# Optimization experiments

Hardware: AMD Instinct MI355X
Metric: run time of the kernel (lower is better)

## Reference

```python
import jax, jax.numpy as jnp
import numpy as np

H_NODE = 256
H_EDGE = 64
B = 8        # number of graphs
A_PER = 64   # anchors per graph
N_PER = 512  # nodes per graph
INF = 1000000.0
EPS = 1e-8
D_MIN, D_MAX = 0.0, 20.0  # _rbf defaults (gvp-style)


def setup_inputs() -> dict:
    key = jax.random.key(0)
    ks = jax.random.split(key, 16)
    h, he = H_NODE, H_EDGE
    n = lambda k, shp, s=1.0: jax.random.normal(k, shp, jnp.float32) * s
    return {
        "anchor_x": n(ks[0], (B * A_PER, 3), 10.0),
        "node_x": n(ks[1], (B * N_PER, 3), 10.0),
        "anchor_features": n(ks[2], (B * A_PER, h)),
        "node_features": n(ks[3], (B * N_PER, h)),
        "batch": jnp.repeat(jnp.arange(B, dtype=jnp.int32), N_PER),
        "anchor_batch": jnp.repeat(jnp.arange(B, dtype=jnp.int32), A_PER),
        "node_mask": (jax.random.uniform(ks[4], (B * N_PER,)) < 0.9).astype(jnp.float32),
        "Wq": n(ks[5], (h, h), h ** -0.5), "bq": jnp.zeros((h,), jnp.float32),
        "Wkv": n(ks[6], (2 * h, h + he), (h + he) ** -0.5), "bkv": jnp.zeros((2 * h,), jnp.float32),
        "ln1_g": jnp.ones((h,), jnp.float32), "ln1_b": jnp.zeros((h,), jnp.float32),
        "W1": n(ks[7], (2 * h, h), h ** -0.5), "b1": jnp.zeros((2 * h,), jnp.float32),
        "W2": n(ks[8], (2 * h, 2 * h), (2 * h) ** -0.5), "b2": jnp.zeros((2 * h,), jnp.float32),
        "W3": n(ks[9], (h, 2 * h), (2 * h) ** -0.5), "b3": jnp.zeros((h,), jnp.float32),
        "ln2_g": jnp.ones((h,), jnp.float32), "ln2_b": jnp.zeros((h,), jnp.float32),
    }


def _ln(x, g, b, eps=1e-5):
    m = x.mean(-1, keepdims=True)
    v = ((x - m) ** 2).mean(-1, keepdims=True)
    return (x - m) * jax.lax.rsqrt(v + eps) * g + b


def _forward(anchor_x, node_x, anchor_features, node_features, node_mask,
             Wq, bq, Wkv, bkv, ln1_g, ln1_b, W1, b1, W2, b2, W3, b3, ln2_g, ln2_b):
    h, he = H_NODE, H_EDGE
    # equal-sized graphs: reshape global tensors to [B, ., .] (batch ids are repeat(arange(B)))
    q = (anchor_features @ Wq.T + bq).reshape(B, A_PER, h)
    ax = anchor_x.reshape(B, A_PER, 3)
    nx = node_x.reshape(B, N_PER, 3)
    nf = node_features.reshape(B, N_PER, h)
    mask = node_mask.reshape(B, N_PER)

    # pairwise anchor->node distances; original adds scalar eps to the diff vector before the norm
    dist = jnp.linalg.norm(ax[:, :, None, :] - nx[:, None, :, :] + EPS, axis=-1)  # [B,A,N]

    # RBF featurization of dist/10 with D_count = h_edge
    mu = jnp.linspace(D_MIN, D_MAX, he)
    sigma = (D_MAX - D_MIN) / he
    rbf = jnp.exp(-(((dist / 10.0)[..., None] - mu) / sigma) ** 2)  # [B,A,N,he]

    # kv_node(cat([node_feat, rbf])) decomposed: node part computed once per node
    Wkv_n, Wkv_e = Wkv[:, :h], Wkv[:, h:]
    kv_n = nf @ Wkv_n.T + bkv                 # [B,N,2h]
    kv_e = rbf @ Wkv_e.T                      # [B,A,N,2h]
    kv = kv_n[:, None, :, :] + kv_e           # [B,A,N,2h]
    k, v = kv[..., :h], kv[..., h:]

    attn = jnp.einsum('bah,banh->ban', q, k)
    attn = attn * ((mask[:, None, :] - 1.0) * INF)  # faithful to original (multiplicative mask)
    attn = jax.nn.softmax(attn, axis=-1)
    upd = jnp.einsum('ban,banh->bah', attn, v).reshape(B * A_PER, h)

    af = _ln(anchor_features + upd, ln1_g, ln1_b)
    m = jax.nn.relu(af @ W1.T + b1)
    m = jax.nn.relu(m @ W2.T + b2)
    m = m @ W3.T + b3
    return _ln(af + m, ln2_g, ln2_b)


def reference(anchor_x, node_x, anchor_features, node_features, batch, anchor_batch, node_mask,
              Wq, bq, Wkv, bkv, ln1_g, ln1_b, W1, b1, W2, b2, W3, b3, ln2_g, ln2_b):
    # batch / anchor_batch encode equal-sized contiguous graphs; structure is baked into reshapes
    return _forward(anchor_x, node_x, anchor_features, node_features, node_mask,
                    Wq, bq, Wkv, bkv, ln1_g, ln1_b, W1, b1, W2, b2, W3, b3, ln2_g, ln2_b)
```

## Files before the change

kernel.cpp:

```cpp
#include <hip/hip_runtime.h>

#define H    256
#define HE   64
#define NPB  512
#define NA   512
#define MU_STEP (20.0f / 63.0f)
#define INV_SIG 3.2f
#define NF_LD4 65

__device__ __forceinline__ float wave_sum(float v) {
#pragma unroll
    for (int o = 32; o; o >>= 1) v += __shfl_xor(v, o, 64);
    return v;
}
__device__ __forceinline__ float wave_max(float v) {
#pragma unroll
    for (int o = 32; o; o >>= 1) v = fmaxf(v, __shfl_xor(v, o, 64));
    return v;
}
__device__ __forceinline__ float block_sum512(float v, float* red8, int t) {
    v = wave_sum(v);
    if ((t & 63) == 0) red8[t >> 6] = v;
    __syncthreads();
    v = red8[0] + red8[1] + red8[2] + red8[3]
      + red8[4] + red8[5] + red8[6] + red8[7];
    __syncthreads();
    return v;
}

__global__ void __launch_bounds__(512) fused_all(
    const float* __restrict__ anchor_x, const float* __restrict__ node_x,
    const float* __restrict__ anchor_f, const float* __restrict__ node_f,
    const float* __restrict__ node_mask,
    const float* __restrict__ Wq,  const float* __restrict__ bq,
    const float* __restrict__ Wkv, const float* __restrict__ bkv,
    const float* __restrict__ ln1_g, const float* __restrict__ ln1_b,
    const float* __restrict__ W1, const float* __restrict__ b1,
    const float* __restrict__ W2, const float* __restrict__ b2,
    const float* __restrict__ W3, const float* __restrict__ b3,
    const float* __restrict__ g2,  const float* __restrict__ bb2,
    float* __restrict__ out)
{
    const int bid = blockIdx.x;
    const int b  = bid & 7;
    const int pr = bid >> 3;
    const int aA = b * 64 + 2 * pr;
    const int aB = aA + 1;
    const int t  = threadIdx.x;
    const int th = t & 255, h = t >> 8;
    const int wv = t >> 6, l = t & 63;
    const int sub = l >> 4, kc16 = l & 15;

    __shared__ __align__(16) float nf_s[2][16 * NF_LD4 * 4];
    __shared__ __align__(16) float qWe_s[2][324];
    __shared__ float q_s[2][256];
    __shared__ float af_s[2][256];
    __shared__ float d10_s[2][NPB];
    __shared__ float mf_s[NPB];
    __shared__ float lg_s[2][NPB];
    __shared__ float w_s[2][NPB];
    __shared__ float snf_s[2][256], rj_s[2][64];
    __shared__ float red[512], red8[8];
    __shared__ int   idx_s[2][NPB];
    __shared__ int   cnt_s[2];

    if (t < 256) af_s[0][t]  = anchor_f[(size_t)aA * 256 + t];
    else         af_s[1][th] = anchor_f[(size_t)aB * 256 + th];
    if (t < 2) cnt_s[t] = 0;

    {
        float axA0 = anchor_x[3 * aA], axA1 = anchor_x[3 * aA + 1], axA2 = anchor_x[3 * aA + 2];
        float axB0 = anchor_x[3 * aB], axB1 = anchor_x[3 * aB + 1], axB2 = anchor_x[3 * aB + 2];
        int ng = b * NPB + t;
        float nx0 = node_x[3 * ng], nx1 = node_x[3 * ng + 1], nx2 = node_x[3 * ng + 2];
        float dx = axA0 - nx0 + 1e-8f, dy = axA1 - nx1 + 1e-8f, dz = axA2 - nx2 + 1e-8f;
        d10_s[0][t] = sqrtf(dx * dx + dy * dy + dz * dz) * 0.1f;
        dx = axB0 - nx0 + 1e-8f; dy = axB1 - nx1 + 1e-8f; dz = axB2 - nx2 + 1e-8f;
        d10_s[1][t] = sqrtf(dx * dx + dy * dy + dz * dz) * 0.1f;
        mf_s[t] = (node_mask[ng] - 1.0f) * 1000000.0f;
    }
    __syncthreads();

    const float4* src0 = (const float4*)(node_f + (size_t)(b * NPB) * 256);
    float4 rA = src0[t], rB = src0[t + 512];

    for (int pass = 0; pass < 8; ++pass) {
        int m = pass * 32 + wv * 4 + sub;
        const float* wr = Wq + (size_t)m * 256 + kc16;
        float aAc = 0.f, aBc = 0.f;
        for (int u = 0; u < 16; u += 8) {
            float w8[8];
#pragma unroll
            for (int v = 0; v < 8; ++v) w8[v] = wr[(u + v) * 16];
#pragma unroll
            for (int v = 0; v < 8; ++v) {
                int c = kc16 + (u + v) * 16;
                aAc = fmaf(w8[v], af_s[0][c], aAc);
                aBc = fmaf(w8[v], af_s[1][c], aBc);
            }
        }
#pragma unroll
        for (int o = 8; o >= 1; o >>= 1) {
            aAc += __shfl_xor(aAc, o, 64);
            aBc += __shfl_xor(aBc, o, 64);
        }
        if (kc16 == 0) {
            float bv = bq[m];
            q_s[0][m] = aAc + bv;
            q_s[1][m] = aBc + bv;
        }
    }
    __syncthreads();

    if (t < 320) {
        float aAc = 0.f, aBc = 0.f;
        for (int o = 0; o < 256; o += 8) {
            float w8[8];
#pragma unroll
            for (int u = 0; u < 8; ++u) w8[u] = Wkv[(size_t)(o + u) * 320 + t];
#pragma unroll
            for (int u = 0; u < 8; ++u) {
                aAc = fmaf(w8[u], q_s[0][o + u], aAc);
                aBc = fmaf(w8[u], q_s[1][o + u], aBc);
            }
        }
        qWe_s[0][t] = aAc;
        qWe_s[1][t] = aBc;
    }
    const int dA = (t >> 6) * NF_LD4 + (t & 63);
    const int dB = ((t >> 6) + 8) * NF_LD4 + (t & 63);
    {
        float4* dst = (float4*)(nf_s[0]);
        dst[dA] = rA; dst[dB] = rB;
    }
    float qbkA = block_sum512((t < 256) ? q_s[0][t] * bkv[t] : 0.f, red8, t);
    float qbkB = block_sum512((t < 256) ? q_s[1][t] * bkv[t] : 0.f, red8, t);

    const int n16 = t >> 5, kc = t & 31;
    const float4* qwA4 = (const float4*)qWe_s[0];
    const float4* qwB4 = (const float4*)qWe_s[1];
    const float4 q0A = qwA4[2 * kc], q1A = qwA4[2 * kc + 1];
    const float4 q0B = qwB4[2 * kc], q1B = qwB4[2 * kc + 1];
    const float qeA0 = qWe_s[0][256 + 2 * kc], qeA1 = qWe_s[0][257 + 2 * kc];
    const float qeB0 = qWe_s[1][256 + 2 * kc], qeB1 = qWe_s[1][257 + 2 * kc];
    const float mu0 = (2 * kc) * MU_STEP, mu1 = (2 * kc + 1) * MU_STEP;

    for (int tile = 0; tile < 32; ++tile) {
        if (tile < 31) {
            const float4* s2 = (const float4*)(node_f + (size_t)(b * NPB + (tile + 1) * 16) * 256);
            rA = s2[t]; rB = s2[t + 512];
        }

        const float4* nf4 = (const float4*)(nf_s[tile & 1]) + n16 * NF_LD4;
        float4 f0 = nf4[2 * kc], f1 = nf4[2 * kc + 1];
        float sA = q0A.x * f0.x + q0A.y * f0.y + q0A.z * f0.z + q0A.w * f0.w
                 + q1A.x * f1.x + q1A.y * f1.y + q1A.z * f1.z + q1A.w * f1.w;
        float sB = q0B.x * f0.x + q0B.y * f0.y + q0B.z * f0.z + q0B.w * f0.w
                 + q1B.x * f1.x + q1B.y * f1.y + q1B.z * f1.z + q1B.w * f1.w;

        const int n = tile * 16 + n16;
        const float dA10 = d10_s[0][n], dB10 = d10_s[1][n];
        {
            float u = (dA10 - mu0) * INV_SIG; sA = fmaf(qeA0, __expf(-u * u), sA);
            u = (dA10 - mu1) * INV_SIG;       sA = fmaf(qeA1, __expf(-u * u), sA);
            u = (dB10 - mu0) * INV_SIG;       sB = fmaf(qeB0, __expf(-u * u), sB);
            u = (dB10 - mu1) * INV_SIG;       sB = fmaf(qeB1, __expf(-u * u), sB);
        }
#pragma unroll
        for (int o = 1; o < 32; o <<= 1) {
            sA += __shfl_xor(sA, o, 64);
            sB += __shfl_xor(sB, o, 64);
        }
        if (kc == 0) {
            lg_s[0][n] = (sA + qbkA) * mf_s[n];
            lg_s[1][n] = (sB + qbkB) * mf_s[n];
        }

        if (tile < 31) {
            float4* dst = (float4*)(nf_s[(tile + 1) & 1]);
            dst[dA] = rA; dst[dB] = rB;
        }
        __syncthreads();
    }

    float lg0 = lg_s[h][th], lg1 = lg_s[h][th + 256];
    {
        float m = wave_max(fmaxf(lg0, lg1));
        if ((t & 63) == 0) red8[t >> 6] = m;
    }
    __syncthreads();
    float gm = fmaxf(fmaxf(red8[4 * h], red8[4 * h + 1]),
                     fmaxf(red8[4 * h + 2], red8[4 * h + 3]));
    __syncthreads();
    float e0 = __expf(lg0 - gm), e1 = __expf(lg1 - gm);
    w_s[h][th] = e0; w_s[h][th + 256] = e1;
    {
        float sm = wave_sum(e0 + e1);
        if ((t & 63) == 0) red8[t >> 6] = sm;
    }
    __syncthreads();
    float inv = 1.0f / (red8[4 * h] + red8[4 * h + 1] + red8[4 * h + 2] + red8[4 * h + 3]);

    if (e0 > 0.f) { int p = atomicAdd(&cnt_s[h], 1); idx_s[h][p] = th; }
    if (e1 > 0.f) { int p = atomicAdd(&cnt_s[h], 1); idx_s[h][p] = th + 256; }
    __syncthreads();
    const int cnt = cnt_s[h];

    {
        float s = 0.f;
        const float* base = node_f + (size_t)(b * NPB) * 256 + th;
        for (int i = 0; i < cnt; ++i) {
            int n = idx_s[h][i];
            s += w_s[h][n] * base[(size_t)n * 256];
        }
        snf_s[h][th] = s;
    }
    {
        int j = th & 63, g = th >> 6;
        float mu = j * MU_STEP;
        float r = 0.f;
        for (int i = g; i < cnt; i += 4) {
            int n = idx_s[h][i];
            float uu = (d10_s[h][n] - mu) * INV_SIG;
            r += w_s[h][n] * __expf(-uu * uu);
        }
        red[t] = r;
    }
    __syncthreads();
    if (th < 64)
        rj_s[h][th] = red[h * 256 + th] + red[h * 256 + th + 64]
                    + red[h * 256 + th + 128] + red[h * 256 + th + 192];
    __syncthreads();

    for (int pass = 0; pass < 8; ++pass) {
        int m = pass * 32 + wv * 4 + sub;
        const float* wr = Wkv + (size_t)(256 + m) * 320 + kc16;
        float aAc = 0.f, aBc = 0.f;
        for (int u = 0; u < 16; u += 8) {
            float w8[8];
#pragma unroll
            for (int v = 0; v < 8; ++v) w8[v] = wr[(u + v) * 16];
#pragma unroll
            for (int v = 0; v < 8; ++v) {
                int c = kc16 + (u + v) * 16;
                aAc = fmaf(w8[v], snf_s[0][c], aAc);
                aBc = fmaf(w8[v], snf_s[1][c], aBc);
            }
        }
        {
            float w4r[4];
#pragma unroll
            for (int v = 0; v < 4; ++v) w4r[v] = wr[256 + v * 16];
#pragma unroll
            for (int v = 0; v < 4; ++v) {
                int j = kc16 + v * 16;
                aAc = fmaf(w4r[v], rj_s[0][j], aAc);
                aBc = fmaf(w4r[v], rj_s[1][j], aBc);
            }
        }
#pragma unroll
        for (int o = 8; o >= 1; o >>= 1) {
            aAc += __shfl_xor(aAc, o, 64);
            aBc += __shfl_xor(aBc, o, 64);
        }
        if (kc16 == 0) { red[m] = aAc; red[256 + m] = aBc; }
    }
    __syncthreads();

    float x = af_s[h][th] + red[h * 256 + th] * inv + bkv[256 + th];
    {
        float s1 = wave_sum(x);
        if ((t & 63) == 0) red8[t >> 6] = s1;
    }
    __syncthreads();
    float mean = (red8[4 * h] + red8[4 * h + 1] + red8[4 * h + 2] + red8[4 * h + 3]) * (1.0f / 256.0f);
    __syncthreads();
    float xc = x - mean;
    {
        float v1 = wave_sum(xc * xc);
        if ((t & 63) == 0) red8[t >> 6] = v1;
    }
    __syncthreads();
    float var = (red8[4 * h] + red8[4 * h + 1] + red8[4 * h + 2] + red8[4 * h + 3]) * (1.0f / 256.0f);
    __syncthreads();
    af_s[h][th] = xc * rsqrtf(var + 1e-5f) * ln1_g[th] + ln1_b[th];
    __syncthreads();

    float* mlp = (float*)nf_s;
    for (int pass = 0; pass < 16; ++pass) {
        int m = pass * 32 + wv * 4 + sub;
        const float* wr = W1 + (size_t)m * 256 + kc16;
        float aAc = 0.f, aBc = 0.f;
        for (int u = 0; u < 16; u += 8) {
            float w8[8];
#pragma unroll
            for (int v = 0; v < 8; ++v) w8[v] = wr[(u + v) * 16];
#pragma unroll
            for (int v = 0; v < 8; ++v) {
                int c = kc16 + (u + v) * 16;
                aAc = fmaf(w8[v], af_s[0][c], aAc);
                aBc = fmaf(w8[v], af_s[1][c], aBc);
            }
        }
#pragma unroll
        for (int o = 8; o >= 1; o >>= 1) {
            aAc += __shfl_xor(aAc, o, 64);
            aBc += __shfl_xor(aBc, o, 64);
        }
        if (kc16 == 0) {
            float bv = b1[m];
            mlp[m]       = fmaxf(aAc + bv, 0.f);
            mlp[512 + m] = fmaxf(aBc + bv, 0.f);
        }
    }
    __syncthreads();

    for (int pass = 0; pass < 16; ++pass) {
        int m = pass * 32 + wv * 4 + sub;
        const float* wr = W2 + (size_t)m * 512 + kc16;
        float aAc = 0.f, aBc = 0.f;
        for (int u = 0; u < 32; u += 8) {
            float w8[8];
#pragma unroll
            for (int v = 0; v < 8; ++v) w8[v] = wr[(u + v) * 16];
#pragma unroll
            for (int v = 0; v < 8; ++v) {
                int c = kc16 + (u + v) * 16;
                aAc = fmaf(w8[v], mlp[c], aAc);
                aBc = fmaf(w8[v], mlp[512 + c], aBc);
            }
        }
#pragma unroll
        for (int o = 8; o >= 1; o >>= 1) {
            aAc += __shfl_xor(aAc, o, 64);
            aBc += __shfl_xor(aBc, o, 64);
        }
        if (kc16 == 0) {
            float bv = b2[m];
            mlp[1024 + m] = fmaxf(aAc + bv, 0.f);
            mlp[1536 + m] = fmaxf(aBc + bv, 0.f);
        }
    }
    __syncthreads();

    for (int pass = 0; pass < 8; ++pass) {
        int m = pass * 32 + wv * 4 + sub;
        const float* wr = W3 + (size_t)m * 512 + kc16;
        float aAc = 0.f, aBc = 0.f;
        for (int u = 0; u < 32; u += 8) {
            float w8[8];
#pragma unroll
            for (int v = 0; v < 8; ++v) w8[v] = wr[(u + v) * 16];
#pragma unroll
            for (int v = 0; v < 8; ++v) {
                int c = kc16 + (u + v) * 16;
                aAc = fmaf(w8[v], mlp[1024 + c], aAc);
                aBc = fmaf(w8[v], mlp[1536 + c], aBc);
            }
        }
#pragma unroll
        for (int o = 8; o >= 1; o >>= 1) {
            aAc += __shfl_xor(aAc, o, 64);
            aBc += __shfl_xor(aBc, o, 64);
        }
        if (kc16 == 0) {
            float bv = b3[m];
            red[m]       = aAc + bv;
            red[256 + m] = aBc + bv;
        }
    }
    __syncthreads();

    const int kh = t >> 8;
    float yA = 0.f, yB = 0.f, gv = 0.f, bv2 = 0.f;
    if (kh == 0) {
        yA = red[th] + af_s[0][th];
        yB = red[256 + th] + af_s[1][th];
        gv = g2[th]; bv2 = bb2[th];
    }
    {
        float s  = block_sum512((kh == 0) ? yA : 0.f, red8, t);
        float mn = s * (1.0f / 256.0f);
        float yc = (kh == 0) ? (yA - mn) : 0.f;
        float vr = block_sum512(yc * yc, red8, t) * (1.0f / 256.0f);
        if (kh == 0)
            out[(size_t)aA * 256 + th] = yc * rsqrtf(vr + 1e-5f) * gv + bv2;
    }
    {
        float s  = block_sum512((kh == 0) ? yB : 0.f, red8, t);
        float mn = s * (1.0f / 256.0f);
        float yc = (kh == 0) ? (yB - mn) : 0.f;
        float vr = block_sum512(yc * yc, red8, t) * (1.0f / 256.0f);
        if (kh == 0)
            out[(size_t)aB * 256 + th] = yc * rsqrtf(vr + 1e-5f) * gv + bv2;
    }
}

extern "C" void kernel_launch(void* const* d_in, const int* in_sizes, int n_in,
                              void* d_out, int out_size, void* d_ws, size_t ws_size,
                              hipStream_t stream)
{
    const float* anchor_x  = (const float*)d_in[0];
    const float* node_x    = (const float*)d_in[1];
    const float* anchor_f  = (const float*)d_in[2];
    const float* node_f    = (const float*)d_in[3];
    const float* node_mask = (const float*)d_in[6];
    const float* Wq        = (const float*)d_in[7];
    const float* bq        = (const float*)d_in[8];
    const float* Wkv       = (const float*)d_in[9];
    const float* bkv       = (const float*)d_in[10];
    const float* ln1_g     = (const float*)d_in[11];
    const float* ln1_b     = (const float*)d_in[12];
    const float* W1        = (const float*)d_in[13];
    const float* b1        = (const float*)d_in[14];
    const float* W2        = (const float*)d_in[15];
    const float* b2        = (const float*)d_in[16];
    const float* W3        = (const float*)d_in[17];
    const float* b3        = (const float*)d_in[18];
    const float* ln2_g     = (const float*)d_in[19];
    const float* ln2_b     = (const float*)d_in[20];

    fused_all<<<256, 512, 0, stream>>>(anchor_x, node_x, anchor_f, node_f,
                                       node_mask, Wq, bq, Wkv, bkv,
                                       ln1_g, ln1_b, W1, b1, W2, b2, W3, b3,
                                       ln2_g, ln2_b, (float*)d_out);
}
```

Measured before the change: 172.9 us.

## Double block size to 1024 threads and stream node features directly from global

Raises the block from 512 to 1024 threads and redistributes every phase (Wq, Wkv projections, logits, softmax, weighted sums, MLP, layernorms) across 16 waves, halving the pass count per GEMV. The logit loop drops the shared-memory double-buffered node-feature tile and instead has each wave read one node row per iteration from global with a register prefetch, doing a full 64-lane shuffle reduction. The MLP intermediates move to dedicated shared arrays. This aims for more parallelism per block, at the cost of more registers per thread, more idle threads in some phases, and uncoalesced-per-wave node loads that rely on cache.

```diff
diff --git a/kernel.cpp b/kernel.cpp
--- a/kernel.cpp
+++ b/kernel.cpp
@@ -6,7 +6,6 @@
 #define NA   512
 #define MU_STEP (20.0f / 63.0f)
 #define INV_SIG 3.2f
-#define NF_LD4 65
 
 __device__ __forceinline__ float wave_sum(float v) {
 #pragma unroll
@@ -18,17 +17,18 @@
     for (int o = 32; o; o >>= 1) v = fmaxf(v, __shfl_xor(v, o, 64));
     return v;
 }
-__device__ __forceinline__ float block_sum512(float v, float* red8, int t) {
+__device__ __forceinline__ float block_sum1024(float v, float* red16, int t) {
     v = wave_sum(v);
-    if ((t & 63) == 0) red8[t >> 6] = v;
-    __syncthreads();
-    v = red8[0] + red8[1] + red8[2] + red8[3]
-      + red8[4] + red8[5] + red8[6] + red8[7];
+    if ((t & 63) == 0) red16[t >> 6] = v;
+    __syncthreads();
+    v = 0.f;
+#pragma unroll
+    for (int i = 0; i < 16; ++i) v += red16[i];
     __syncthreads();
     return v;
 }
 
-__global__ void __launch_bounds__(512) fused_all(
+__global__ void __launch_bounds__(1024) fused_all(
     const float* __restrict__ anchor_x, const float* __restrict__ node_x,
     const float* __restrict__ anchor_f, const float* __restrict__ node_f,
     const float* __restrict__ node_mask,
@@ -47,11 +47,9 @@
     const int aA = b * 64 + 2 * pr;
     const int aB = aA + 1;
     const int t  = threadIdx.x;
-    const int th = t & 255, h = t >> 8;
     const int wv = t >> 6, l = t & 63;
     const int sub = l >> 4, kc16 = l & 15;
 
-    __shared__ __align__(16) float nf_s[2][16 * NF_LD4 * 4];
     __shared__ __align__(16) float qWe_s[2][324];
     __shared__ float q_s[2][256];
     __shared__ float af_s[2][256];
@@ -60,15 +58,16 @@
     __shared__ float lg_s[2][NPB];
     __shared__ float w_s[2][NPB];
     __shared__ float snf_s[2][256], rj_s[2][64];
-    __shared__ float red[512], red8[8];
+    __shared__ float m1_s[2][512], m2_s[2][512];
+    __shared__ float red[512], red16[16];
     __shared__ int   idx_s[2][NPB];
     __shared__ int   cnt_s[2];
 
-    if (t < 256) af_s[0][t]  = anchor_f[(size_t)aA * 256 + t];
-    else         af_s[1][th] = anchor_f[(size_t)aB * 256 + th];
+    if (t < 256)       af_s[0][t]        = anchor_f[(size_t)aA * 256 + t];
+    else if (t < 512)  af_s[1][t - 256]  = anchor_f[(size_t)aB * 256 + (t - 256)];
     if (t < 2) cnt_s[t] = 0;
 
-    {
+    if (t < 512) {
         float axA0 = anchor_x[3 * aA], axA1 = anchor_x[3 * aA + 1], axA2 = anchor_x[3 * aA + 2];
         float axB0 = anchor_x[3 * aB], axB1 = anchor_x[3 * aB + 1], axB2 = anchor_x[3 * aB + 2];
         int ng = b * NPB + t;
@@ -81,11 +80,9 @@
     }
     __syncthreads();
 
-    const float4* src0 = (const float4*)(node_f + (size_t)(b * NPB) * 256);
-    float4 rA = src0[t], rB = src0[t + 512];
-
-    for (int pass = 0; pass < 8; ++pass) {
-        int m = pass * 32 + wv * 4 + sub;
+#pragma unroll
+    for (int pass = 0; pass < 4; ++pass) {
+        int m = pass * 64 + wv * 4 + sub;
         const float* wr = Wq + (size_t)m * 256 + kc16;
         float aAc = 0.f, aBc = 0.f;
         for (int u = 0; u < 16; u += 8) {
@@ -112,128 +109,117 @@
     }
     __syncthreads();
 
-    if (t < 320) {
-        float aAc = 0.f, aBc = 0.f;
-        for (int o = 0; o < 256; o += 8) {
-            float w8[8];
-#pragma unroll
-            for (int u = 0; u < 8; ++u) w8[u] = Wkv[(size_t)(o + u) * 320 + t];
-#pragma unroll
-            for (int u = 0; u < 8; ++u) {
-                aAc = fmaf(w8[u], q_s[0][o + u], aAc);
-                aBc = fmaf(w8[u], q_s[1][o + u], aBc);
-            }
-        }
-        qWe_s[0][t] = aAc;
-        qWe_s[1][t] = aBc;
-    }
-    const int dA = (t >> 6) * NF_LD4 + (t & 63);
-    const int dB = ((t >> 6) + 8) * NF_LD4 + (t & 63);
-    {
-        float4* dst = (float4*)(nf_s[0]);
-        dst[dA] = rA; dst[dB] = rB;
-    }
-    float qbkA = block_sum512((t < 256) ? q_s[0][t] * bkv[t] : 0.f, red8, t);
-    float qbkB = block_sum512((t < 256) ? q_s[1][t] * bkv[t] : 0.f, red8, t);
-
-    const int n16 = t >> 5, kc = t & 31;
-    const float4* qwA4 = (const float4*)qWe_s[0];
-    const float4* qwB4 = (const float4*)qWe_s[1];
-    const float4 q0A = qwA4[2 * kc], q1A = qwA4[2 * kc + 1];
-    const float4 q0B = qwB4[2 * kc], q1B = qwB4[2 * kc + 1];
-    const float qeA0 = qWe_s[0][256 + 2 * kc], qeA1 = qWe_s[0][257 + 2 * kc];
-    const float qeB0 = qWe_s[1][256 + 2 * kc], qeB1 = qWe_s[1][257 + 2 * kc];
-    const float mu0 = (2 * kc) * MU_STEP, mu1 = (2 * kc + 1) * MU_STEP;
-
-    for (int tile = 0; tile < 32; ++tile) {
-        if (tile < 31) {
-            const float4* s2 = (const float4*)(node_f + (size_t)(b * NPB + (tile + 1) * 16) * 256);
-            rA = s2[t]; rB = s2[t + 512];
-        }
-
-        const float4* nf4 = (const float4*)(nf_s[tile & 1]) + n16 * NF_LD4;
-        float4 f0 = nf4[2 * kc], f1 = nf4[2 * kc + 1];
-        float sA = q0A.x * f0.x + q0A.y * f0.y + q0A.z * f0.z + q0A.w * f0.w
-                 + q1A.x * f1.x + q1A.y * f1.y + q1A.z * f1.z + q1A.w * f1.w;
-        float sB = q0B.x * f0.x + q0B.y * f0.y + q0B.z * f0.z + q0B.w * f0.w
-                 + q1B.x * f1.x + q1B.y * f1.y + q1B.z * f1.z + q1B.w * f1.w;
-
-        const int n = tile * 16 + n16;
-        const float dA10 = d10_s[0][n], dB10 = d10_s[1][n];
-        {
-            float u = (dA10 - mu0) * INV_SIG; sA = fmaf(qeA0, __expf(-u * u), sA);
-            u = (dA10 - mu1) * INV_SIG;       sA = fmaf(qeA1, __expf(-u * u), sA);
-            u = (dB10 - mu0) * INV_SIG;       sB = fmaf(qeB0, __expf(-u * u), sB);
-            u = (dB10 - mu1) * INV_SIG;       sB = fmaf(qeB1, __expf(-u * u), sB);
-        }
-#pragma unroll
-        for (int o = 1; o < 32; o <<= 1) {
-            sA += __shfl_xor(sA, o, 64);
-            sB += __shfl_xor(sB, o, 64);
-        }
-        if (kc == 0) {
-            lg_s[0][n] = (sA + qbkA) * mf_s[n];
-            lg_s[1][n] = (sB + qbkB) * mf_s[n];
-        }
-
-        if (tile < 31) {
-            float4* dst = (float4*)(nf_s[(tile + 1) & 1]);
-            dst[dA] = rA; dst[dB] = rB;
-        }
-        __syncthreads();
-    }
-
-    float lg0 = lg_s[h][th], lg1 = lg_s[h][th + 256];
-    {
-        float m = wave_max(fmaxf(lg0, lg1));
-        if ((t & 63) == 0) red8[t >> 6] = m;
-    }
-    __syncthreads();
-    float gm = fmaxf(fmaxf(red8[4 * h], red8[4 * h + 1]),
-                     fmaxf(red8[4 * h + 2], red8[4 * h + 3]));
-    __syncthreads();
-    float e0 = __expf(lg0 - gm), e1 = __expf(lg1 - gm);
-    w_s[h][th] = e0; w_s[h][th + 256] = e1;
-    {
-        float sm = wave_sum(e0 + e1);
-        if ((t & 63) == 0) red8[t >> 6] = sm;
-    }
-    __syncthreads();
-    float inv = 1.0f / (red8[4 * h] + red8[4 * h + 1] + red8[4 * h + 2] + red8[4 * h + 3]);
-
-    if (e0 > 0.f) { int p = atomicAdd(&cnt_s[h], 1); idx_s[h][p] = th; }
-    if (e1 > 0.f) { int p = atomicAdd(&cnt_s[h], 1); idx_s[h][p] = th + 256; }
-    __syncthreads();
-    const int cnt = cnt_s[h];
-
-    {
+    {
+        int ha = -1, col = 0;
+        if (t < 320)                   { ha = 0; col = t; }
+        else if (t >= 512 && t < 832)  { ha = 1; col = t - 512; }
+        if (ha >= 0) {
+            const float* qs = q_s[ha];
+            float acc = 0.f;
+            for (int o = 0; o < 256; o += 8) {
+                float w8[8];
+#pragma unroll
+                for (int u = 0; u < 8; ++u) w8[u] = Wkv[(size_t)(o + u) * 320 + col];
+#pragma unroll
+                for (int u = 0; u < 8; ++u) acc = fmaf(w8[u], qs[o + u], acc);
+            }
+            qWe_s[ha][col] = acc;
+        }
+    }
+    float qbkA = block_sum1024((t < 256) ? q_s[0][t] * bkv[t] : 0.f, red16, t);
+    float qbkB = block_sum1024((t < 256) ? q_s[1][t] * bkv[t] : 0.f, red16, t);
+
+    {
+        const float4 qA = ((const float4*)qWe_s[0])[l];
+        const float4 qB = ((const float4*)qWe_s[1])[l];
+        const float qeA = qWe_s[0][256 + l], qeB = qWe_s[1][256 + l];
+        const float muL = l * MU_STEP;
+        const float4* nfb = (const float4*)(node_f + (size_t)(b * NPB) * 256);
+
+        float4 f = nfb[(size_t)wv * 64 + l];
+        for (int it = 0; it < 32; ++it) {
+            const int n = wv + it * 16;
+            float4 fn;
+            if (it < 31) fn = nfb[(size_t)(n + 16) * 64 + l];
+
+            float sA = qA.x * f.x + qA.y * f.y + qA.z * f.z + qA.w * f.w;
+            float sB = qB.x * f.x + qB.y * f.y + qB.z * f.z + qB.w * f.w;
+            float dA10 = d10_s[0][n], dB10 = d10_s[1][n];
+            float u = (dA10 - muL) * INV_SIG; sA = fmaf(qeA, __expf(-u * u), sA);
+            u = (dB10 - muL) * INV_SIG;       sB = fmaf(qeB, __expf(-u * u), sB);
+#pragma unroll
+            for (int o = 1; o < 64; o <<= 1) {
+                sA += __shfl_xor(sA, o, 64);
+                sB += __shfl_xor(sB, o, 64);
+            }
+            if (l == 0) {
+                lg_s[0][n] = (sA + qbkA) * mf_s[n];
+                lg_s[1][n] = (sB + qbkB) * mf_s[n];
+            }
+            f = fn;
+        }
+    }
+    __syncthreads();
+
+    const int h8 = t >> 9, n9 = t & 511;
+    float lg = lg_s[h8][n9];
+    {
+        float m = wave_max(lg);
+        if (l == 0) red16[wv] = m;
+    }
+    __syncthreads();
+    float gmA = red16[0], gmB = red16[8];
+#pragma unroll
+    for (int i = 1; i < 8; ++i) { gmA = fmaxf(gmA, red16[i]); gmB = fmaxf(gmB, red16[8 + i]); }
+    __syncthreads();
+    float e = __expf(lg - (h8 ? gmB : gmA));
+    w_s[h8][n9] = e;
+    {
+        float sm = wave_sum(e);
+        if (l == 0) red16[wv] = sm;
+    }
+    __syncthreads();
+    float smA = 0.f, smB = 0.f;
+#pragma unroll
+    for (int i = 0; i < 8; ++i) { smA += red16[i]; smB += red16[8 + i]; }
+    const float invA = 1.0f / smA, invB = 1.0f / smB;
+    if (e > 0.f) { int p = atomicAdd(&cnt_s[h8], 1); idx_s[h8][p] = n9; }
+    __syncthreads();
+
+    if (t < 512) {
+        const int h = t >> 8, col = t & 255;
+        const int cnt = cnt_s[h];
         float s = 0.f;
-        const float* base = node_f + (size_t)(b * NPB) * 256 + th;
+        const float* base = node_f + (size_t)(b * NPB) * 256 + col;
         for (int i = 0; i < cnt; ++i) {
             int n = idx_s[h][i];
             s += w_s[h][n] * base[(size_t)n * 256];
         }
-        snf_s[h][th] = s;
-    }
-    {
-        int j = th & 63, g = th >> 6;
+        snf_s[h][col] = s;
+    } else {
+        const int tt = t - 512;
+        const int ha = tt >> 8, j = tt & 63, g = (tt >> 6) & 3;
+        const int cnt = cnt_s[ha];
         float mu = j * MU_STEP;
         float r = 0.f;
         for (int i = g; i < cnt; i += 4) {
-            int n = idx_s[h][i];
-            float uu = (d10_s[h][n] - mu) * INV_SIG;
-            r += w_s[h][n] * __expf(-uu * uu);
-        }
-        red[t] = r;
-    }
-    __syncthreads();
-    if (th < 64)
-        rj_s[h][th] = red[h * 256 + th] + red[h * 256 + th + 64]
-                    + red[h * 256 + th + 128] + red[h * 256 + th + 192];
-    __syncthreads();
-
-    for (int pass = 0; pass < 8; ++pass) {
-        int m = pass * 32 + wv * 4 + sub;
+            int n = idx_s[ha][i];
+            float uu = (d10_s[ha][n] - mu) * INV_SIG;
+            r += w_s[ha][n] * __expf(-uu * uu);
+        }
+        red[tt] = r;
+    }
+    __syncthreads();
+    if (t < 128) {
+        int ha = t >> 6, j = t & 63;
+        rj_s[ha][j] = red[ha * 256 + j] + red[ha * 256 + 64 + j]
+                    + red[ha * 256 + 128 + j] + red[ha * 256 + 192 + j];
+    }
+    __syncthreads();
+
+#pragma unroll
+    for (int pass = 0; pass < 4; ++pass) {
+        int m = pass * 64 + wv * 4 + sub;
         const float* wr = Wkv + (size_t)(256 + m) * 320 + kc16;
         float aAc = 0.f, aBc = 0.f;
         for (int u = 0; u < 16; u += 8) {
@@ -267,28 +253,34 @@
     }
     __syncthreads();
 
-    float x = af_s[h][th] + red[h * 256 + th] * inv + bkv[256 + th];
+    const int h = (t >> 8) & 1, th = t & 255;
+    float x = 0.f;
+    if (t < 512)
+        x = af_s[h][th] + red[h * 256 + th] * (h ? invB : invA) + bkv[256 + th];
     {
         float s1 = wave_sum(x);
-        if ((t & 63) == 0) red8[t >> 6] = s1;
-    }
-    __syncthreads();
-    float mean = (red8[4 * h] + red8[4 * h + 1] + red8[4 * h + 2] + red8[4 * h + 3]) * (1.0f / 256.0f);
-    __syncthreads();
-    float xc = x - mean;
+        if (l == 0) red16[wv] = s1;
+    }
+    __syncthreads();
+    float meanA = (red16[0] + red16[1] + red16[2] + red16[3]) * (1.0f / 256.0f);
+    float meanB = (red16[4] + red16[5] + red16[6] + red16[7]) * (1.0f / 256.0f);
+    __syncthreads();
+    float xc = (t < 512) ? (x - (h ? meanB : meanA)) : 0.f;
     {
         float v1 = wave_sum(xc * xc);
-        if ((t & 63) == 0) red8[t >> 6] = v1;
-    }
-    __syncthreads();
-    float var = (red8[4 * h] + red8[4 * h + 1] + red8[4 * h + 2] + red8[4 * h + 3]) * (1.0f / 256.0f);
-    __syncthreads();
-    af_s[h][th] = xc * rsqrtf(var + 1e-5f) * ln1_g[th] + ln1_b[th];
-    __syncthreads();
-
-    float* mlp = (float*)nf_s;
-    for (int pass = 0; pass < 16; ++pass) {
-        int m = pass * 32 + wv * 4 + sub;
+        if (l == 0) red16[wv] = v1;
+    }
+    __syncthreads();
+    float varA = (red16[0] + red16[1] + red16[2] + red16[3]) * (1.0f / 256.0f);
+    float varB = (red16[4] + red16[5] + red16[6] + red16[7]) * (1.0f / 256.0f);
+    __syncthreads();
+    if (t < 512)
+        af_s[h][th] = xc * rsqrtf((h ? varB : varA) + 1e-5f) * ln1_g[th] + ln1_b[th];
+    __syncthreads();
+
+#pragma unroll
+    for (int pass = 0; pass < 8; ++pass) {
+        int m = pass * 64 + wv * 4 + sub;
         const float* wr = W1 + (size_t)m * 256 + kc16;
         float aAc = 0.f, aBc = 0.f;
         for (int u = 0; u < 16; u += 8) {
@@ -309,14 +301,15 @@
         }
         if (kc16 == 0) {
             float bv = b1[m];
-            mlp[m]       = fmaxf(aAc + bv, 0.f);
-            mlp[512 + m] = fmaxf(aBc + bv, 0.f);
-        }
-    }
-    __syncthreads();
-
-    for (int pass = 0; pass < 16; ++pass) {
-        int m = pass * 32 + wv * 4 + sub;
+            m1_s[0][m] = fmaxf(aAc + bv, 0.f);
+            m1_s[1][m] = fmaxf(aBc + bv, 0.f);
+        }
+    }
+    __syncthreads();
+
+#pragma unroll
+    for (int pass = 0; pass < 8; ++pass) {
+        int m = pass * 64 + wv * 4 + sub;
         const float* wr = W2 + (size_t)m * 512 + kc16;
         float aAc = 0.f, aBc = 0.f;
         for (int u = 0; u < 32; u += 8) {
@@ -326,8 +319,8 @@
 #pragma unroll
             for (int v = 0; v < 8; ++v) {
                 int c = kc16 + (u + v) * 16;
-                aAc = fmaf(w8[v], mlp[c], aAc);
-                aBc = fmaf(w8[v], mlp[512 + c], aBc);
+                aAc = fmaf(w8[v], m1_s[0][c], aAc);
+                aBc = fmaf(w8[v], m1_s[1][c], aBc);
             }
         }
 #pragma unroll
@@ -337,14 +330,15 @@
         }
         if (kc16 == 0) {
             float bv = b2[m];
-            mlp[1024 + m] = fmaxf(aAc + bv, 0.f);
-            mlp[1536 + m] = fmaxf(aBc + bv, 0.f);
-        }
-    }
-    __syncthreads();
-
-    for (int pass = 0; pass < 8; ++pass) {
-        int m = pass * 32 + wv * 4 + sub;
+            m2_s[0][m] = fmaxf(aAc + bv, 0.f);
+            m2_s[1][m] = fmaxf(aBc + bv, 0.f);
+        }
+    }
+    __syncthreads();
+
+#pragma unroll
+    for (int pass = 0; pass < 4; ++pass) {
+        int m = pass * 64 + wv * 4 + sub;
         const float* wr = W3 + (size_t)m * 512 + kc16;
         float aAc = 0.f, aBc = 0.f;
         for (int u = 0; u < 32; u += 8) {
@@ -354,8 +348,8 @@
 #pragma unroll
             for (int v = 0; v < 8; ++v) {
                 int c = kc16 + (u + v) * 16;
-                aAc = fmaf(w8[v], mlp[1024 + c], aAc);
-                aBc = fmaf(w8[v], mlp[1536 + c], aBc);
+                aAc = fmaf(w8[v], m2_s[0][c], aAc);
+                aBc = fmaf(w8[v], m2_s[1][c], aBc);
             }
         }
 #pragma unroll
@@ -371,28 +365,28 @@
     }
     __syncthreads();
 
-    const int kh = t >> 8;
-    float yA = 0.f, yB = 0.f, gv = 0.f, bv2 = 0.f;
-    if (kh == 0) {
-        yA = red[th] + af_s[0][th];
-        yB = red[256 + th] + af_s[1][th];
-        gv = g2[th]; bv2 = bb2[th];
-    }
-    {
-        float s  = block_sum512((kh == 0) ? yA : 0.f, red8, t);
-        float mn = s * (1.0f / 256.0f);
-        float yc = (kh == 0) ? (yA - mn) : 0.f;
-        float vr = block_sum512(yc * yc, red8, t) * (1.0f / 256.0f);
-        if (kh == 0)
-            out[(size_t)aA * 256 + th] = yc * rsqrtf(vr + 1e-5f) * gv + bv2;
-    }
-    {
-        float s  = block_sum512((kh == 0) ? yB : 0.f, red8, t);
-        float mn = s * (1.0f / 256.0f);
-        float yc = (kh == 0) ? (yB - mn) : 0.f;
-        float vr = block_sum512(yc * yc, red8, t) * (1.0f / 256.0f);
-        if (kh == 0)
-            out[(size_t)aB * 256 + th] = yc * rsqrtf(vr + 1e-5f) * gv + bv2;
+    float y = 0.f;
+    if (t < 512) y = red[h * 256 + th] + af_s[h][th];
+    {
+        float s1 = wave_sum(y);
+        if (l == 0) red16[wv] = s1;
+    }
+    __syncthreads();
+    float mnA = (red16[0] + red16[1] + red16[2] + red16[3]) * (1.0f / 256.0f);
+    float mnB = (red16[4] + red16[5] + red16[6] + red16[7]) * (1.0f / 256.0f);
+    __syncthreads();
+    float yc = (t < 512) ? (y - (h ? mnB : mnA)) : 0.f;
+    {
+        float v1 = wave_sum(yc * yc);
+        if (l == 0) red16[wv] = v1;
+    }
+    __syncthreads();
+    float vrA = (red16[0] + red16[1] + red16[2] + red16[3]) * (1.0f / 256.0f);
+    float vrB = (red16[4] + red16[5] + red16[6] + red16[7]) * (1.0f / 256.0f);
+    if (t < 512) {
+        int aOut = h ? aB : aA;
+        out[(size_t)aOut * 256 + th] =
+            yc * rsqrtf((h ? vrB : vrA) + 1e-5f) * g2[th] + bb2[th];
     }
 }
 
@@ -420,8 +414,8 @@
     const float* ln2_g     = (const float*)d_in[19];
     const float* ln2_b     = (const float*)d_in[20];
 
-    fused_all<<<256, 512, 0, stream>>>(anchor_x, node_x, anchor_f, node_f,
-                                       node_mask, Wq, bq, Wkv, bkv,
-                                       ln1_g, ln1_b, W1, b1, W2, b2, W3, b3,
-                                       ln2_g, ln2_b, (float*)d_out);
+    fused_all<<<256, 1024, 0, stream>>>(anchor_x, node_x, anchor_f, node_f,
+                                        node_mask, Wq, bq, Wkv, bkv,
+                                        ln1_g, ln1_b, W1, b1, W2, b2, W3, b3,
+                                        ln2_g, ln2_b, (float*)d_out);
 }
```

Result: faster. 166.2 us (-3.9%).
